# Performance work log

Hardware: AMD Instinct MI355X
Metric: run time of the kernel (lower is better)

Reference implementation:

```python
import jax, jax.numpy as jnp
import numpy as np

D_MODEL = 1024
NUM_HEADS = 16
D_HEAD = D_MODEL // NUM_HEADS
B, T = 2, 2048


def setup_inputs() -> dict:
    key = jax.random.key(0)
    kx, kq, kk, kv, ko = jax.random.split(key, 5)
    # xavier_uniform bound for square (D,D) linear weights
    bound = float(np.sqrt(6.0 / (D_MODEL + D_MODEL)))
    uni = lambda k: jax.random.uniform(k, (D_MODEL, D_MODEL), jnp.float32, -bound, bound)
    return {
        "x": jax.random.normal(kx, (B, T, D_MODEL), jnp.float32),
        "Wq": uni(kq),
        "Wk": uni(kk),
        "Wv": uni(kv),
        "Wo": uni(ko),
    }


def _split_heads(x):
    # (B, T, D) -> (B, H, T, d_head)
    b, t, _ = x.shape
    return x.reshape(b, t, NUM_HEADS, D_HEAD).transpose(0, 2, 1, 3)


def _exclusive_output_mod(Y, V):
    dt = V.dtype
    tiny = jnp.asarray(jnp.finfo(dt).tiny, dt)
    eps = jnp.asarray(jnp.finfo(dt).eps, dt)
    v_sq = jnp.sum(V * V, axis=-1, keepdims=True)
    y_dot_v = jnp.sum(Y * V, axis=-1, keepdims=True)
    scale = jnp.where(v_sq > 0, y_dot_v / jnp.maximum(v_sq, tiny), jnp.zeros_like(y_dot_v))
    Z = Y - scale * V
    residual_norm = jnp.linalg.norm(Z, axis=-1, keepdims=True)
    reference_norm = jnp.maximum(
        jnp.linalg.norm(Y, axis=-1, keepdims=True),
        jnp.linalg.norm(V, axis=-1, keepdims=True),
    )
    cleanup_tol = eps * Z.shape[-1] * reference_norm
    return jnp.where((v_sq > 0) & (residual_norm <= cleanup_tol), jnp.zeros_like(Z), Z)


def reference(x, Wq, Wk, Wv, Wo):
    Q = _split_heads(x @ Wq.T)  # (B,H,T,dh)
    K = _split_heads(x @ Wk.T)
    V = _split_heads(x @ Wv.T)
    sm_scale = 1.0 / np.sqrt(D_HEAD)
    scores = jnp.einsum("bhqd,bhkd->bhqk", Q, K) * sm_scale
    P = jax.nn.softmax(scores, axis=-1)
    Y = jnp.einsum("bhqk,bhkd->bhqd", P, V)
    Z = _exclusive_output_mod(Y, V)
    # merge heads: (B,H,T,dh) -> (B,T,D)
    Zm = Z.transpose(0, 2, 1, 3).reshape(x.shape[0], x.shape[1], D_MODEL)
    return Zm @ Wo.T
```

## Files before the change

### kernel.cpp

```cpp
#include <hip/hip_runtime.h>
#include <math.h>

#define DM   1024
#define TTOK 2048
#define NTOK 4096

typedef __bf16 bf16x8 __attribute__((ext_vector_type(8)));
typedef __bf16 bf16x4 __attribute__((ext_vector_type(4)));
typedef __bf16 bf16x2 __attribute__((ext_vector_type(2)));
typedef float  f32x4  __attribute__((ext_vector_type(4)));
typedef float  f32x16 __attribute__((ext_vector_type(16)));

#define QSCALE 0.18033688011112042f

#if defined(__has_builtin)
#if __has_builtin(__builtin_amdgcn_exp2f)
#define EXP2F(x) __builtin_amdgcn_exp2f(x)
#endif
#endif
#ifndef EXP2F
#define EXP2F(x) exp2f(x)
#endif

#define GLDS16(g, l) __builtin_amdgcn_global_load_lds( \
    (__attribute__((address_space(1))) void*)(g),      \
    (__attribute__((address_space(3))) void*)(l), 16, 0, 0)

__device__ __forceinline__ unsigned pk2(float a, float b) {
    bf16x2 t; t[0] = (__bf16)a; t[1] = (__bf16)b;
    return __builtin_bit_cast(unsigned, t);
}
union FU { unsigned u[4]; bf16x8 v; };

__global__ __launch_bounds__(256)
void cvt_all(const float* __restrict__ x,  const float* __restrict__ Wq,
             const float* __restrict__ Wk, const float* __restrict__ Wv,
             const float* __restrict__ Wo, __bf16* __restrict__ dst) {
    size_t g = ((size_t)blockIdx.x * 256 + threadIdx.x) * 8;
    const float* s;
    size_t off;
    const size_t NX = (size_t)NTOK * DM;
    if (g < NX) { s = x; off = g; }
    else {
        size_t gg = g - NX;
        int w = (int)(gg >> 20);
        off = gg & ((1u << 20) - 1);
        s = (w == 0) ? Wq : (w == 1) ? Wk : (w == 2) ? Wv : Wo;
    }
    float4 a = *(const float4*)(s + off);
    float4 b = *(const float4*)(s + off + 4);
    bf16x8 v;
    v[0] = (__bf16)a.x; v[1] = (__bf16)a.y; v[2] = (__bf16)a.z; v[3] = (__bf16)a.w;
    v[4] = (__bf16)b.x; v[5] = (__bf16)b.y; v[6] = (__bf16)b.z; v[7] = (__bf16)b.w;
    *(bf16x8*)(dst + g) = v;
}

#define LSTR 136
#define DBUF 8192

__global__ __launch_bounds__(256)
void gemm_qkv(const __bf16* __restrict__ X,
              const __bf16* __restrict__ W0, const __bf16* __restrict__ W1,
              const __bf16* __restrict__ W2,
              __bf16* __restrict__ Oq, __bf16* __restrict__ Ok,
              __bf16* __restrict__ Ovt)
{
    const int z = blockIdx.z;
    const __bf16 *A, *B;
    int m0, n0;
    if (z < 2) {
        A = z ? W1 : W0; B = X;
        m0 = blockIdx.y * 128; n0 = blockIdx.x * 128;
    } else {
        A = X; B = W2;
        m0 = blockIdx.x * 128; n0 = blockIdx.y * 128;
    }

    __shared__ __attribute__((aligned(16))) __bf16 smem[128 * LSTR];

    const int tid  = threadIdx.x;
    const int lane = tid & 63;
    const int wave = tid >> 6;
    const int wm = wave & 1, wn = wave >> 1;
    const int col = lane & 15, quad = lane >> 4;

    const __bf16* Ag = A + (size_t)(m0 + (tid >> 2)) * DM + (tid & 3) * 8;
    const __bf16* Bg = B + (size_t)(n0 + (tid >> 2)) * DM + (tid & 3) * 8;
    __bf16* lA = smem + tid * 8;
    __bf16* lB = smem + 4096 + tid * 8;

    f32x4 acc[4][4];
#pragma unroll
    for (int i = 0; i < 4; ++i)
#pragma unroll
        for (int j = 0; j < 4; ++j)
#pragma unroll
            for (int r = 0; r < 4; ++r) acc[i][j][r] = 0.0f;

    GLDS16(Ag,                   lA);
    GLDS16(Ag + (size_t)64 * DM, lA + 2048);
    GLDS16(Bg,                   lB);
    GLDS16(Bg + (size_t)64 * DM, lB + 2048);
    __syncthreads();

    const int nk = DM / 32;
    for (int t = 0; t < nk; ++t) {
        const int cur = (t & 1) * DBUF;
        const int nxt = DBUF - cur;

        if (t + 1 < nk) {
            const int k1 = (t + 1) * 32;
            GLDS16(Ag + k1,                   lA + nxt);
            GLDS16(Ag + (size_t)64 * DM + k1, lA + nxt + 2048);
            GLDS16(Bg + k1,                   lB + nxt);
            GLDS16(Bg + (size_t)64 * DM + k1, lB + nxt + 2048);
        }

        const __bf16* Asr = smem + cur;
        const __bf16* Bsr = smem + cur + 4096;
        bf16x8 af[4], bfr[4];
#pragma unroll
        for (int i = 0; i < 4; ++i)
            af[i] = *(const bf16x8*)&Asr[(wm * 64 + i * 16 + col) * 32 + quad * 8];
#pragma unroll
        for (int j = 0; j < 4; ++j)
            bfr[j] = *(const bf16x8*)&Bsr[(wn * 64 + j * 16 + col) * 32 + quad * 8];
#pragma unroll
        for (int i = 0; i < 4; ++i)
#pragma unroll
            for (int j = 0; j < 4; ++j)
                acc[i][j] = __builtin_amdgcn_mfma_f32_16x16x32_bf16(af[i], bfr[j], acc[i][j], 0, 0, 0);

        __syncthreads();
    }

    const float sc = (z == 0) ? QSCALE : 1.0f;
#pragma unroll
    for (int i = 0; i < 4; ++i)
#pragma unroll
        for (int j = 0; j < 4; ++j) {
            const int ml = wm * 64 + i * 16 + quad * 4;
            const int nl = wn * 64 + j * 16 + col;
            bf16x4 pk;
#pragma unroll
            for (int r = 0; r < 4; ++r) pk[r] = (__bf16)(acc[i][j][r] * sc);
            *(bf16x4*)&smem[nl * LSTR + ml] = pk;
        }
    __syncthreads();

#pragma unroll
    for (int it = 0; it < 8; ++it) {
        int c   = tid + 256 * it;
        int row = c >> 4;
        int ch  = (c & 15) * 8;
        bf16x8 v = *(const bf16x8*)&smem[row * LSTR + ch];
        if (z < 2) {
            int t  = n0 + row;
            int b  = t >> 11; t &= 2047;
            int hd = m0 + ch;
            int h  = hd >> 6, d = hd & 63;
            *(bf16x8*)&((z ? Ok : Oq)[(((size_t)(b * 16 + h)) * TTOK + t) * 64 + d]) = v;
        } else {
            int hd = n0 + row;
            int h  = hd >> 6, d = hd & 63;
            int t  = m0 + ch;
            int b  = t >> 11; t &= 2047;
            *(bf16x8*)&Ovt[(((size_t)(b * 16 + h)) * 64 + d) * TTOK + t] = v;
        }
    }
}

#define ODBUF 6144

__global__ __launch_bounds__(256)
void gemm_oproj(const __bf16* __restrict__ X, const __bf16* __restrict__ Wo,
                float* __restrict__ Of)
{
    const int f = blockIdx.x + 8 * blockIdx.y;
    const int c = f & 7, i0 = f >> 3;
    const int m0 = (8 * c + (i0 & 7)) * 64;
    const int n0 = (i0 >> 3) * 128;

    __shared__ __attribute__((aligned(16))) __bf16 smem[2 * ODBUF];

    const int tid  = threadIdx.x;
    const int lane = tid & 63;
    const int wave = tid >> 6;
    const int col = lane & 15, quad = lane >> 4;

    const __bf16* Ag = X  + (size_t)(m0 + (tid >> 2)) * DM + (tid & 3) * 8;
    const __bf16* Bg = Wo + (size_t)(n0 + (tid >> 2)) * DM + (tid & 3) * 8;
    __bf16* lA = smem + tid * 8;
    __bf16* lB = smem + 2048 + tid * 8;

    f32x4 acc[4][2];
#pragma unroll
    for (int i = 0; i < 4; ++i)
#pragma unroll
        for (int j = 0; j < 2; ++j)
#pragma unroll
            for (int r = 0; r < 4; ++r) acc[i][j][r] = 0.0f;

    GLDS16(Ag,                   lA);
    GLDS16(Bg,                   lB);
    GLDS16(Bg + (size_t)64 * DM, lB + 2048);
    __syncthreads();

    const int nk = DM / 32;
    for (int t = 0; t < nk; ++t) {
        const int cur = (t & 1) * ODBUF;
        const int nxt = ODBUF - cur;
        if (t + 1 < nk) {
            const int k1 = (t + 1) * 32;
            GLDS16(Ag + k1,                   lA + nxt);
            GLDS16(Bg + k1,                   lB + nxt);
            GLDS16(Bg + (size_t)64 * DM + k1, lB + nxt + 2048);
        }
        const __bf16* Asr = smem + cur;
        const __bf16* Bsr = smem + cur + 2048;
        bf16x8 af[4], bfr[2];
#pragma unroll
        for (int i = 0; i < 4; ++i)
            af[i] = *(const bf16x8*)&Asr[(i * 16 + col) * 32 + quad * 8];
#pragma unroll
        for (int j = 0; j < 2; ++j)
            bfr[j] = *(const bf16x8*)&Bsr[(wave * 32 + j * 16 + col) * 32 + quad * 8];
#pragma unroll
        for (int i = 0; i < 4; ++i)
#pragma unroll
            for (int j = 0; j < 2; ++j)
                acc[i][j] = __builtin_amdgcn_mfma_f32_16x16x32_bf16(af[i], bfr[j], acc[i][j], 0, 0, 0);
        __syncthreads();
    }

#pragma unroll
    for (int i = 0; i < 4; ++i)
#pragma unroll
        for (int j = 0; j < 2; ++j) {
            const int mb = m0 + i * 16 + quad * 4;
            const int n  = n0 + wave * 32 + j * 16 + col;
#pragma unroll
            for (int r = 0; r < 4; ++r)
                Of[(size_t)(mb + r) * DM + n] = acc[i][j][r];
        }
}

__global__ __launch_bounds__(512)
__attribute__((amdgpu_waves_per_eu(4)))
void attn_mfma(const __bf16* __restrict__ Qg, const __bf16* __restrict__ Kg,
               const __bf16* __restrict__ Vtg, __bf16* __restrict__ Zm)
{
    const int bh = blockIdx.y;
    const int q0 = blockIdx.x * 128;
    const size_t base = (size_t)bh * TTOK * 64;

    __shared__ __attribute__((aligned(16))) __bf16 lds[2][2][2][64 * 72];

    const int tid  = threadIdx.x;
    const int lane = tid & 63;
    const int wave = tid >> 6;
    const int half = wave >> 2;
    const int qw   = wave & 3;
    const int c32  = lane & 31, h32 = lane >> 5;

    bf16x8 qf[4];
    const __bf16* qrow = Qg + base + (size_t)(q0 + qw * 32 + c32) * 64 + h32 * 8;
#pragma unroll
    for (int st = 0; st < 4; ++st)
        qf[st] = *(const bf16x8*)(qrow + st * 16);

    f32x16 O[2];
#pragma unroll
    for (int r = 0; r < 16; ++r) { O[0][r] = 0.0f; O[1][r] = 0.0f; }
    float lsum = 0.0f;

    const int tid8 = tid & 255;
    const int rs   = tid8 >> 2;
    const int soff = (tid8 & 3) * 16;
    const int kb0  = half * 1024;

    {
        const __bf16* kp = Kg  + base + (size_t)(kb0 + rs) * 64 + soff;
        const __bf16* vp = Vtg + base + (size_t)rs * TTOK + kb0 + soff;
        bf16x8 k0 = *(const bf16x8*)(kp);
        bf16x8 k1 = *(const bf16x8*)(kp + 8);
        bf16x8 v0 = *(const bf16x8*)(vp);
        bf16x8 v1 = *(const bf16x8*)(vp + 8);
        *(bf16x8*)&lds[half][0][0][rs * 72 + soff]     = k0;
        *(bf16x8*)&lds[half][0][0][rs * 72 + soff + 8] = k1;
        *(bf16x8*)&lds[half][1][0][rs * 72 + soff]     = v0;
        *(bf16x8*)&lds[half][1][0][rs * 72 + soff + 8] = v1;
    }
    bf16x8 kr0, kr1, vr0, vr1;
    {
        const __bf16* kp = Kg  + base + (size_t)(kb0 + 64 + rs) * 64 + soff;
        const __bf16* vp = Vtg + base + (size_t)rs * TTOK + kb0 + 64 + soff;
        kr0 = *(const bf16x8*)(kp); kr1 = *(const bf16x8*)(kp + 8);
        vr0 = *(const bf16x8*)(vp); vr1 = *(const bf16x8*)(vp + 8);
    }
    __syncthreads();

    for (int it = 0; it < 16; ++it) {
        const int cur = it & 1;
        const __bf16* Kc = &lds[half][0][cur][0];
        const __bf16* Vc = &lds[half][1][cur][0];

        f32x16 s0, s1;
#pragma unroll
        for (int r = 0; r < 16; ++r) { s0[r] = 0.0f; s1[r] = 0.0f; }
#pragma unroll
        for (int st = 0; st < 4; ++st) {
            bf16x8 a0 = *(const bf16x8*)&Kc[(c32)      * 72 + h32 * 8 + st * 16];
            bf16x8 a1 = *(const bf16x8*)&Kc[(32 + c32) * 72 + h32 * 8 + st * 16];
            s0 = __builtin_amdgcn_mfma_f32_32x32x16_bf16(a0, qf[st], s0, 0, 0, 0);
            s1 = __builtin_amdgcn_mfma_f32_32x32x16_bf16(a1, qf[st], s1, 0, 0, 0);
        }

#pragma unroll
        for (int ks = 0; ks < 4; ++ks) {
            const f32x16& sv = (ks & 2) ? s1 : s0;
            const int rb = (ks & 1) * 8;
            float p0 = EXP2F(sv[rb + 0]), p1 = EXP2F(sv[rb + 1]);
            float p2 = EXP2F(sv[rb + 2]), p3 = EXP2F(sv[rb + 3]);
            float p4 = EXP2F(sv[rb + 4]), p5 = EXP2F(sv[rb + 5]);
            float p6 = EXP2F(sv[rb + 6]), p7 = EXP2F(sv[rb + 7]);
            lsum += ((p0 + p1) + (p2 + p3)) + ((p4 + p5) + (p6 + p7));
            unsigned A0 = pk2(p0, p1), A1 = pk2(p2, p3);
            unsigned B0 = pk2(p4, p5), B1 = pk2(p6, p7);
            unsigned s0w = h32 ? A0 : B0;
            unsigned s1w = h32 ? A1 : B1;
            unsigned r0 = __shfl_xor(s0w, 32, 64);
            unsigned r1 = __shfl_xor(s1w, 32, 64);
            FU fu;
            fu.u[0] = h32 ? r0 : A0;
            fu.u[1] = h32 ? r1 : A1;
            fu.u[2] = h32 ? B0 : r0;
            fu.u[3] = h32 ? B1 : r1;
            bf16x8 v0 = *(const bf16x8*)&Vc[(c32)      * 72 + h32 * 8 + ks * 16];
            bf16x8 v1 = *(const bf16x8*)&Vc[(32 + c32) * 72 + h32 * 8 + ks * 16];
            O[0] = __builtin_amdgcn_mfma_f32_32x32x16_bf16(v0, fu.v, O[0], 0, 0, 0);
            O[1] = __builtin_amdgcn_mfma_f32_32x32x16_bf16(v1, fu.v, O[1], 0, 0, 0);
        }

        *(bf16x8*)&lds[half][0][cur ^ 1][rs * 72 + soff]     = kr0;
        *(bf16x8*)&lds[half][0][cur ^ 1][rs * 72 + soff + 8] = kr1;
        *(bf16x8*)&lds[half][1][cur ^ 1][rs * 72 + soff]     = vr0;
        *(bf16x8*)&lds[half][1][cur ^ 1][rs * 72 + soff + 8] = vr1;

        {
            int itn = (it + 2) & 15;
            const __bf16* kp = Kg  + base + (size_t)(kb0 + itn * 64 + rs) * 64 + soff;
            const __bf16* vp = Vtg + base + (size_t)rs * TTOK + kb0 + itn * 64 + soff;
            kr0 = *(const bf16x8*)(kp); kr1 = *(const bf16x8*)(kp + 8);
            vr0 = *(const bf16x8*)(vp); vr1 = *(const bf16x8*)(vp + 8);
        }

        __syncthreads();
    }

    float* cb = (float*)&lds[0][0][0][0];
    if (wave >= 4) {
        float* me = cb + qw * 2048;
#pragma unroll
        for (int r = 0; r < 16; ++r) {
            me[r * 64 + lane]        = O[0][r];
            me[(16 + r) * 64 + lane] = O[1][r];
        }
        cb[8192 + qw * 64 + lane] = lsum;
    }
    __syncthreads();
    if (wave >= 4) return;
    {
        const float* pr = cb + qw * 2048;
#pragma unroll
        for (int r = 0; r < 16; ++r) {
            O[0][r] += pr[r * 64 + lane];
            O[1][r] += pr[(16 + r) * 64 + lane];
        }
        lsum += cb[8192 + qw * 64 + lane];
    }
    const float ltot = lsum + __shfl_xor(lsum, 32, 64);
    const float inv  = 1.0f / ltot;

    const int q = q0 + qw * 32 + c32;
    float vq[2][16];
#pragma unroll
    for (int db = 0; db < 2; ++db)
#pragma unroll
        for (int rg = 0; rg < 16; ++rg) {
            int d = db * 32 + (rg & 3) + 8 * (rg >> 2) + 4 * h32;
            vq[db][rg] = (float)Vtg[base + (size_t)d * TTOK + q];
        }

    const int b = bh >> 4, h = bh & 15;
    float y[2][16];
    float yv = 0.f, v2 = 0.f, yy = 0.f;
#pragma unroll
    for (int db = 0; db < 2; ++db)
#pragma unroll
        for (int rg = 0; rg < 16; ++rg) {
            float yval = O[db][rg] * inv;
            float vval = vq[db][rg];
            y[db][rg] = yval;
            yv += yval * vval; v2 += vval * vval; yy += yval * yval;
        }
    yv += __shfl_xor(yv, 32, 64);
    v2 += __shfl_xor(v2, 32, 64);
    yy += __shfl_xor(yy, 32, 64);
    float scl = (v2 > 0.0f) ? yv / fmaxf(v2, 1.1754943508222875e-38f) : 0.0f;
    float zz = 0.f;
    float zvv[2][16];
#pragma unroll
    for (int db = 0; db < 2; ++db)
#pragma unroll
        for (int rg = 0; rg < 16; ++rg) {
            zvv[db][rg] = y[db][rg] - scl * vq[db][rg];
            zz += zvv[db][rg] * zvv[db][rg];
        }
    zz += __shfl_xor(zz, 32, 64);
    float znorm = sqrtf(zz);
    float refn  = fmaxf(sqrtf(yy), sqrtf(v2));
    bool  wipe  = (v2 > 0.0f) && (znorm <= 1.1920928955078125e-07f * 64.0f * refn);
#pragma unroll
    for (int db = 0; db < 2; ++db)
#pragma unroll
        for (int g = 0; g < 4; ++g) {
            bf16x4 pk;
#pragma unroll
            for (int r = 0; r < 4; ++r)
                pk[r] = (__bf16)(wipe ? 0.0f : zvv[db][4 * g + r]);
            int d = db * 32 + 8 * g + 4 * h32;
            *(bf16x4*)&Zm[((size_t)(b * TTOK + q)) * DM + h * 64 + d] = pk;
        }
}

extern "C" void kernel_launch(void* const* d_in, const int* in_sizes, int n_in,
                              void* d_out, int out_size, void* d_ws, size_t ws_size,
                              hipStream_t stream) {
    const float* x  = (const float*)d_in[0];
    const float* Wq = (const float*)d_in[1];
    const float* Wk = (const float*)d_in[2];
    const float* Wv = (const float*)d_in[3];
    const float* Wo = (const float*)d_in[4];

    const size_t NX = (size_t)NTOK * DM;
    const size_t NW = (size_t)DM * DM;
    __bf16* xb  = (__bf16*)d_ws;
    __bf16* wqb = xb  + NX;
    __bf16* wkb = wqb + NW;
    __bf16* wvb = wkb + NW;
    __bf16* wob = wvb + NW;
    __bf16* Qb  = wob + NW;
    __bf16* Kb  = Qb  + NX;
    __bf16* Vtb = Kb  + NX;
    __bf16* Zmb = Vtb + NX;

    cvt_all<<<(NX + 4 * NW) / 2048, 256, 0, stream>>>(x, Wq, Wk, Wv, Wo, xb);

    gemm_qkv<<<dim3(32, 8, 3), 256, 0, stream>>>(
        xb, wqb, wkb, wvb, Qb, Kb, Vtb);

    attn_mfma<<<dim3(TTOK / 128, 32), 512, 0, stream>>>(Qb, Kb, Vtb, Zmb);

    gemm_oproj<<<dim3(8, 64), 256, 0, stream>>>(Zmb, wob, (float*)d_out);
}
```

Baseline: 185.2 us.

## Triple-buffer LDS in QKV and output projection GEMMs with partial vmcnt waits

Both projection GEMMs move from a double-buffered LDS pipeline with a full __syncthreads per k-step to a three-stage ring buffer. Loads run two k-tiles ahead, and each step waits only for the oldest tile's loads using inline s_waitcnt vmcnt(N) plus s_barrier. The goal is to hide global-to-LDS latency better and avoid draining all outstanding loads every iteration. In exchange it uses more LDS per block, which may reduce occupancy. The hand-written waitcnt also relies on exact load counting, and with a single barrier per step a buffer could in principle be overwritten while a slow wave is still reading it.

New measurement: 179.7 us, median of 2. 1.03x faster.

```diff
diff --git a/kernel.cpp b/kernel.cpp
--- a/kernel.cpp
+++ b/kernel.cpp
@@ -25,6 +25,8 @@
 #define GLDS16(g, l) __builtin_amdgcn_global_load_lds( \
     (__attribute__((address_space(1))) void*)(g),      \
     (__attribute__((address_space(3))) void*)(l), 16, 0, 0)
+
+#define WB(N) asm volatile("s_waitcnt vmcnt(" #N ") lgkmcnt(0)\n\ts_barrier" ::: "memory")
 
 __device__ __forceinline__ unsigned pk2(float a, float b) {
     bf16x2 t; t[0] = (__bf16)a; t[1] = (__bf16)b;
@@ -76,7 +78,7 @@
         m0 = blockIdx.x * 128; n0 = blockIdx.y * 128;
     }
 
-    __shared__ __attribute__((aligned(16))) __bf16 smem[128 * LSTR];
+    __shared__ __attribute__((aligned(16))) __bf16 smem[3 * DBUF];
 
     const int tid  = threadIdx.x;
     const int lane = tid & 63;
@@ -86,8 +88,31 @@
 
     const __bf16* Ag = A + (size_t)(m0 + (tid >> 2)) * DM + (tid & 3) * 8;
     const __bf16* Bg = B + (size_t)(n0 + (tid >> 2)) * DM + (tid & 3) * 8;
-    __bf16* lA = smem + tid * 8;
-    __bf16* lB = smem + 4096 + tid * 8;
+    const int lo = tid * 8;
+
+#define QSTAGE(d, k) do {                                            \
+        GLDS16(Ag + (k) * 32,                   (d) + lo);           \
+        GLDS16(Ag + (size_t)64 * DM + (k) * 32, (d) + lo + 2048);    \
+        GLDS16(Bg + (k) * 32,                   (d) + 4096 + lo);    \
+        GLDS16(Bg + (size_t)64 * DM + (k) * 32, (d) + 4096 + lo + 2048); \
+    } while (0)
+
+#define QCOMP(p) do {                                                        \
+        const __bf16* Asr = (p);                                             \
+        const __bf16* Bsr = (p) + 4096;                                     \
+        bf16x8 af[4], bfr[4];                                                \
+        _Pragma("unroll")                                                    \
+        for (int i = 0; i < 4; ++i)                                          \
+            af[i] = *(const bf16x8*)&Asr[(wm * 64 + i * 16 + col) * 32 + quad * 8]; \
+        _Pragma("unroll")                                                    \
+        for (int j = 0; j < 4; ++j)                                          \
+            bfr[j] = *(const bf16x8*)&Bsr[(wn * 64 + j * 16 + col) * 32 + quad * 8]; \
+        _Pragma("unroll")                                                    \
+        for (int i = 0; i < 4; ++i)                                          \
+            _Pragma("unroll")                                                \
+            for (int j = 0; j < 4; ++j)                                      \
+                acc[i][j] = __builtin_amdgcn_mfma_f32_16x16x32_bf16(af[i], bfr[j], acc[i][j], 0, 0, 0); \
+    } while (0)
 
     f32x4 acc[4][4];
 #pragma unroll
@@ -97,43 +122,22 @@
 #pragma unroll
             for (int r = 0; r < 4; ++r) acc[i][j][r] = 0.0f;
 
-    GLDS16(Ag,                   lA);
-    GLDS16(Ag + (size_t)64 * DM, lA + 2048);
-    GLDS16(Bg,                   lB);
-    GLDS16(Bg + (size_t)64 * DM, lB + 2048);
+    __bf16 *b0 = smem, *b1 = smem + DBUF, *b2 = smem + 2 * DBUF;
+
+    QSTAGE(b0, 0);
+    QSTAGE(b1, 1);
+
+    const int nk = DM / 32;
+    for (int t = 0; t < nk - 1; ++t) {
+        WB(4);
+        if (t + 2 < nk) QSTAGE(b2, t + 2);
+        QCOMP(b0);
+        __bf16* tmp = b0; b0 = b1; b1 = b2; b2 = tmp;
+    }
+    WB(0);
+    QCOMP(b0);
+
     __syncthreads();
-
-    const int nk = DM / 32;
-    for (int t = 0; t < nk; ++t) {
-        const int cur = (t & 1) * DBUF;
-        const int nxt = DBUF - cur;
-
-        if (t + 1 < nk) {
-            const int k1 = (t + 1) * 32;
-            GLDS16(Ag + k1,                   lA + nxt);
-            GLDS16(Ag + (size_t)64 * DM + k1, lA + nxt + 2048);
-            GLDS16(Bg + k1,                   lB + nxt);
-            GLDS16(Bg + (size_t)64 * DM + k1, lB + nxt + 2048);
-        }
-
-        const __bf16* Asr = smem + cur;
-        const __bf16* Bsr = smem + cur + 4096;
-        bf16x8 af[4], bfr[4];
-#pragma unroll
-        for (int i = 0; i < 4; ++i)
-            af[i] = *(const bf16x8*)&Asr[(wm * 64 + i * 16 + col) * 32 + quad * 8];
-#pragma unroll
-        for (int j = 0; j < 4; ++j)
-            bfr[j] = *(const bf16x8*)&Bsr[(wn * 64 + j * 16 + col) * 32 + quad * 8];
-#pragma unroll
-        for (int i = 0; i < 4; ++i)
-#pragma unroll
-            for (int j = 0; j < 4; ++j)
-                acc[i][j] = __builtin_amdgcn_mfma_f32_16x16x32_bf16(af[i], bfr[j], acc[i][j], 0, 0, 0);
-
-        __syncthreads();
-    }
-
     const float sc = (z == 0) ? QSCALE : 1.0f;
 #pragma unroll
     for (int i = 0; i < 4; ++i)
@@ -168,6 +172,8 @@
             *(bf16x8*)&Ovt[(((size_t)(b * 16 + h)) * 64 + d) * TTOK + t] = v;
         }
     }
+#undef QSTAGE
+#undef QCOMP
 }
 
 #define ODBUF 6144
@@ -181,7 +187,7 @@
     const int m0 = (8 * c + (i0 & 7)) * 64;
     const int n0 = (i0 >> 3) * 128;
 
-    __shared__ __attribute__((aligned(16))) __bf16 smem[2 * ODBUF];
+    __shared__ __attribute__((aligned(16))) __bf16 smem[3 * ODBUF];
 
     const int tid  = threadIdx.x;
     const int lane = tid & 63;
@@ -190,8 +196,30 @@
 
     const __bf16* Ag = X  + (size_t)(m0 + (tid >> 2)) * DM + (tid & 3) * 8;
     const __bf16* Bg = Wo + (size_t)(n0 + (tid >> 2)) * DM + (tid & 3) * 8;
-    __bf16* lA = smem + tid * 8;
-    __bf16* lB = smem + 2048 + tid * 8;
+    const int lo = tid * 8;
+
+#define OSTAGE(d, k) do {                                            \
+        GLDS16(Ag + (k) * 32,                   (d) + lo);           \
+        GLDS16(Bg + (k) * 32,                   (d) + 2048 + lo);    \
+        GLDS16(Bg + (size_t)64 * DM + (k) * 32, (d) + 2048 + lo + 2048); \
+    } while (0)
+
+#define OCOMP(p) do {                                                        \
+        const __bf16* Asr = (p);                                             \
+        const __bf16* Bsr = (p) + 2048;                                     \
+        bf16x8 af[4], bfr[2];                                                \
+        _Pragma("unroll")                                                    \
+        for (int i = 0; i < 4; ++i)                                          \
+            af[i] = *(const bf16x8*)&Asr[(i * 16 + col) * 32 + quad * 8];    \
+        _Pragma("unroll")                                                    \
+        for (int j = 0; j < 2; ++j)                                          \
+            bfr[j] = *(const bf16x8*)&Bsr[(wave * 32 + j * 16 + col) * 32 + quad * 8]; \
+        _Pragma("unroll")                                                    \
+        for (int i = 0; i < 4; ++i)                                          \
+            _Pragma("unroll")                                                \
+            for (int j = 0; j < 2; ++j)                                      \
+                acc[i][j] = __builtin_amdgcn_mfma_f32_16x16x32_bf16(af[i], bfr[j], acc[i][j], 0, 0, 0); \
+    } while (0)
 
     f32x4 acc[4][2];
 #pragma unroll
@@ -201,37 +229,20 @@
 #pragma unroll
             for (int r = 0; r < 4; ++r) acc[i][j][r] = 0.0f;
 
-    GLDS16(Ag,                   lA);
-    GLDS16(Bg,                   lB);
-    GLDS16(Bg + (size_t)64 * DM, lB + 2048);
-    __syncthreads();
+    __bf16 *b0 = smem, *b1 = smem + ODBUF, *b2 = smem + 2 * ODBUF;
+
+    OSTAGE(b0, 0);
+    OSTAGE(b1, 1);
 
     const int nk = DM / 32;
-    for (int t = 0; t < nk; ++t) {
-        const int cur = (t & 1) * ODBUF;
-        const int nxt = ODBUF - cur;
-        if (t + 1 < nk) {
-            const int k1 = (t + 1) * 32;
-            GLDS16(Ag + k1,                   lA + nxt);
-            GLDS16(Bg + k1,                   lB + nxt);
-            GLDS16(Bg + (size_t)64 * DM + k1, lB + nxt + 2048);
-        }
-        const __bf16* Asr = smem + cur;
-        const __bf16* Bsr = smem + cur + 2048;
-        bf16x8 af[4], bfr[2];
-#pragma unroll
-        for (int i = 0; i < 4; ++i)
-            af[i] = *(const bf16x8*)&Asr[(i * 16 + col) * 32 + quad * 8];
-#pragma unroll
-        for (int j = 0; j < 2; ++j)
-            bfr[j] = *(const bf16x8*)&Bsr[(wave * 32 + j * 16 + col) * 32 + quad * 8];
-#pragma unroll
-        for (int i = 0; i < 4; ++i)
-#pragma unroll
-            for (int j = 0; j < 2; ++j)
-                acc[i][j] = __builtin_amdgcn_mfma_f32_16x16x32_bf16(af[i], bfr[j], acc[i][j], 0, 0, 0);
-        __syncthreads();
-    }
+    for (int t = 0; t < nk - 1; ++t) {
+        WB(3);
+        if (t + 2 < nk) OSTAGE(b2, t + 2);
+        OCOMP(b0);
+        __bf16* tmp = b0; b0 = b1; b1 = b2; b2 = tmp;
+    }
+    WB(0);
+    OCOMP(b0);
 
 #pragma unroll
     for (int i = 0; i < 4; ++i)
@@ -243,6 +254,8 @@
             for (int r = 0; r < 4; ++r)
                 Of[(size_t)(mb + r) * DM + n] = acc[i][j][r];
         }
+#undef OSTAGE
+#undef OCOMP
 }
 
 __global__ __launch_bounds__(512)
```
